# Performance work log

Measured on AMD Instinct MI355X. Metric: run time of the kernel, lower is better.

The kernel has to match this reference:

```python
import jax, jax.numpy as jnp
import numpy as np

N, E, D, L = 50000, 400000, 128, 5
EPS = 1e-5  # BatchNorm1d default eps


def setup_inputs() -> dict:
    key = jax.random.key(0)
    ks = jax.random.split(key, 9)
    x = jax.random.normal(ks[0], (N, D), jnp.float32)
    edge_index = jax.random.randint(ks[1], (2, E), 0, N)
    edge_attr = jax.random.normal(ks[2], (E, 4), jnp.float32)
    # per-layer params (stacked over L layers)
    W1 = jax.random.normal(ks[3], (L, 3, D), jnp.float32) * (6.0 / (3 + D)) ** 0.5
    W2 = jax.random.normal(ks[4], (L, 1, D), jnp.float32) * (6.0 / (1 + D)) ** 0.5
    Wm = jax.random.normal(ks[5], (L, D, 2 * D), jnp.float32) * (6.0 / (3 * D)) ** 0.5
    bm = jnp.zeros((L, D), jnp.float32)
    gamma = jnp.ones((L, D), jnp.float32)
    beta = jnp.zeros((L, D), jnp.float32)
    return dict(x=x, edge_index=edge_index, edge_attr=edge_attr,
                W1=W1, W2=W2, Wm=Wm, bm=bm, gamma=gamma, beta=beta)


def reference(x, edge_index, edge_attr, W1, W2, Wm, bm, gamma, beta):
    row, col = edge_index[0], edge_index[1]
    # symmetric GCN norm: deg computed by scattering ones at col
    deg = jax.ops.segment_sum(jnp.ones((E,), x.dtype), col, num_segments=N)
    deg_safe = jnp.where(deg > 0, deg, 1.0)
    dinv = jnp.where(deg > 0, deg_safe ** -0.5, 0.0)  # [N]
    norm = dinv[row] * dinv[col]                      # [E]

    h = x
    for l in range(L):
        # edge feature projection ('2-3d'): first 3 cols @ W1 + last col @ W2
        edge_fea = edge_attr[:, :3] @ W1[l] + edge_attr[:, 3:] @ W2[l]  # [E, D]
        # message: norm * (x_j + edge_fea), gather at source (row)
        msg = norm[:, None] * (h[row] + edge_fea)                       # [E, D]
        # aggregate: scatter-add at target (col)
        agg = jax.ops.segment_sum(msg, col, num_segments=N)             # [N, D]
        # mlp(concat([x, out])) with ReLU
        h2 = jax.nn.relu(jnp.concatenate([h, agg], axis=1) @ Wm[l].T + bm[l])
        # BatchNorm1d (training mode: batch stats, biased variance)
        mean = h2.mean(axis=0)
        var = jnp.mean((h2 - mean) ** 2, axis=0)
        h = gamma[l] * (h2 - mean) * jax.lax.rsqrt(var + EPS) + beta[l]
        if l < L - 1:
            h = jax.nn.relu(h)
        # dropout p=0 -> identity
    return h
```

## Files before the change

### kernel.cpp

```cpp
#include <hip/hip_runtime.h>

#define D 128
#define EPSBN 1e-5f
#define PB 400
#define GROWS 64
#define GBK 64

typedef __attribute__((ext_vector_type(8))) short bf16x8;
typedef __attribute__((ext_vector_type(4))) float f32x4;

static __device__ __forceinline__ unsigned short f2b(float f) {
    unsigned u = __float_as_uint(f);
    unsigned r = u + 0x7FFF + ((u >> 16) & 1);
    return (unsigned short)(r >> 16);
}
static __device__ __forceinline__ float b2f_lo(unsigned p) { return __uint_as_float(p << 16); }
static __device__ __forceinline__ float b2f_hi(unsigned p) { return __uint_as_float(p & 0xFFFF0000u); }

static __device__ __forceinline__ unsigned short f2h(float f) {
    _Float16 h = (_Float16)f;
    unsigned short u;
    __builtin_memcpy(&u, &h, 2);
    return u;
}
static __device__ __forceinline__ float h2f(unsigned short u) {
    _Float16 h;
    __builtin_memcpy(&h, &u, 2);
    return (float)h;
}
static __device__ __forceinline__ float h2f_lo(unsigned p) { return h2f((unsigned short)(p & 0xFFFF)); }
static __device__ __forceinline__ float h2f_hi(unsigned p) { return h2f((unsigned short)(p >> 16)); }


__global__ void k_deg(const int* __restrict__ ei, int E, int* __restrict__ deg,
                      int* __restrict__ pos) {
    int e = blockIdx.x * 256 + threadIdx.x;
    if (e < E) pos[e] = atomicAdd(&deg[ei[E + e]], 1);
}

__global__ void k_bsum(const int* __restrict__ deg, int* __restrict__ bsum, int N) {
    __shared__ int sm[256];
    int t = threadIdx.x, v = blockIdx.x * 256 + t;
    sm[t] = (v < N) ? deg[v] : 0;
    __syncthreads();
    for (int off = 128; off > 0; off >>= 1) {
        if (t < off) sm[t] += sm[t + off];
        __syncthreads();
    }
    if (t == 0) bsum[blockIdx.x] = sm[0];
}

__global__ void k_bscan(const int* __restrict__ bsum, int* __restrict__ boff,
                        int* __restrict__ row_ptr, int NB, int N, int E) {
    __shared__ int sm[256];
    int t = threadIdx.x;
    int v = (t < NB) ? bsum[t] : 0;
    sm[t] = v;
    __syncthreads();
    for (int off = 1; off < 256; off <<= 1) {
        int x = (t >= off) ? sm[t - off] : 0;
        __syncthreads();
        sm[t] += x;
        __syncthreads();
    }
    if (t < NB) boff[t] = sm[t] - v;
    if (t == 0) row_ptr[N] = E;
}

__global__ void k_scatter(const int* __restrict__ deg, const int* __restrict__ boff,
                          int* __restrict__ row_ptr, int N) {
    __shared__ int sm[256];
    int t = threadIdx.x, v = blockIdx.x * 256 + t;
    int val = (v < N) ? deg[v] : 0;
    sm[t] = val;
    __syncthreads();
    for (int off = 1; off < 256; off <<= 1) {
        int x = (t >= off) ? sm[t - off] : 0;
        __syncthreads();
        sm[t] += x;
        __syncthreads();
    }
    if (v < N) row_ptr[v] = boff[blockIdx.x] + sm[t] - val;
}

__global__ void k_place(const int* __restrict__ ei, const int* __restrict__ row_ptr,
                        const int* __restrict__ pos, int2* __restrict__ csr, int E) {
    int e = blockIdx.x * 256 + threadIdx.x;
    if (e >= E) return;
    int c = ei[E + e];
    csr[row_ptr[c] + pos[e]] = make_int2(ei[e], e);
}

__global__ void k_cvals(const int* __restrict__ row_ptr, int2* __restrict__ csr,
                        const int* __restrict__ deg, const float* __restrict__ attr,
                        float4* __restrict__ cvals, int N) {
    int v = blockIdx.x * 256 + threadIdx.x;
    if (v >= N) return;
    int dgv = deg[v];
    float dv = (dgv > 0) ? rsqrtf((float)dgv) : 0.f;
    int jb = row_ptr[v], je = row_ptr[v + 1];
    float4 acc = make_float4(0.f, 0.f, 0.f, 0.f);
    for (int j = jb; j < je; ++j) {
        int2 e = csr[j];
        int dgs = deg[e.x];
        float ds = (dgs > 0) ? rsqrtf((float)dgs) : 0.f;
        float nm = ds * dv;
        float4 a = *(const float4*)(attr + (size_t)e.y * 4);
        acc.x += nm * a.x; acc.y += nm * a.y;
        acc.z += nm * a.z; acc.w += nm * a.w;
        csr[j] = make_int2(e.x, __float_as_int(nm));
    }
    cvals[v] = acc;
}

__global__ void k_cvt(const float* __restrict__ in, unsigned short* __restrict__ outp, int n4) {
    int i = blockIdx.x * 256 + threadIdx.x;
    if (i >= n4) return;
    float4 v = *(const float4*)(in + (size_t)i * 4);
    ushort4 p;
    p.x = f2b(v.x); p.y = f2b(v.y); p.z = f2b(v.z); p.w = f2b(v.w);
    *(ushort4*)(outp + (size_t)i * 4) = p;
}


__global__ __launch_bounds__(256) void k_spmm(
        const unsigned short* __restrict__ hb, const int* __restrict__ row_ptr,
        const int2* __restrict__ csr, const float4* __restrict__ cvals,
        const float* __restrict__ W1l, const float* __restrict__ W2l,
        const float* __restrict__ scsh, int apply,
        unsigned short* __restrict__ aggb, int N) {
    int lane = threadIdx.x & 63;
    int wave = threadIdx.x >> 6;
    int nh = lane >> 5;
    int v = blockIdx.x * 8 + wave * 2 + nh;
    if (v >= N) return;
    int qw = (lane >> 4) & 1;
    int l4 = lane & 15;
    int d0 = l4 * 8;
    int jb = row_ptr[v], je = row_ptr[v + 1];

    float a[8];
#pragma unroll
    for (int i = 0; i < 8; ++i) a[i] = 0.f;

    if (apply) {
        float sc[8], sh[8];
#pragma unroll
        for (int i = 0; i < 8; i += 4) {
            float4 s = *(const float4*)(scsh + d0 + i);
            float4 t = *(const float4*)(scsh + D + d0 + i);
            sc[i] = s.x; sc[i + 1] = s.y; sc[i + 2] = s.z; sc[i + 3] = s.w;
            sh[i] = t.x; sh[i + 1] = t.y; sh[i + 2] = t.z; sh[i + 3] = t.w;
        }
        for (int j0 = jb; j0 < je; j0 += 4) {
            int ja = j0 + qw, jc = j0 + 2 + qw;
            bool oa = (ja < je), oc = (jc < je);
            int2 ea = csr[oa ? ja : jb];
            int2 ec = csr[oc ? jc : jb];
            float na = oa ? __int_as_float(ea.y) : 0.f;
            float nc = oc ? __int_as_float(ec.y) : 0.f;
            uint4 pa = *(const uint4*)(hb + (size_t)ea.x * D + d0);
            uint4 pc = *(const uint4*)(hb + (size_t)ec.x * D + d0);
            float xa[8] = {h2f_lo(pa.x), h2f_hi(pa.x), h2f_lo(pa.y), h2f_hi(pa.y),
                           h2f_lo(pa.z), h2f_hi(pa.z), h2f_lo(pa.w), h2f_hi(pa.w)};
            float xc[8] = {h2f_lo(pc.x), h2f_hi(pc.x), h2f_lo(pc.y), h2f_hi(pc.y),
                           h2f_lo(pc.z), h2f_hi(pc.z), h2f_lo(pc.w), h2f_hi(pc.w)};
#pragma unroll
            for (int i = 0; i < 8; ++i) {
                a[i] += na * fmaxf(sc[i] * xa[i] + sh[i], 0.f);
                a[i] += nc * fmaxf(sc[i] * xc[i] + sh[i], 0.f);
            }
        }
    } else {
        for (int j0 = jb; j0 < je; j0 += 4) {
            int ja = j0 + qw, jc = j0 + 2 + qw;
            bool oa = (ja < je), oc = (jc < je);
            int2 ea = csr[oa ? ja : jb];
            int2 ec = csr[oc ? jc : jb];
            float na = oa ? __int_as_float(ea.y) : 0.f;
            float nc = oc ? __int_as_float(ec.y) : 0.f;
            uint4 pa = *(const uint4*)(hb + (size_t)ea.x * D + d0);
            uint4 pc = *(const uint4*)(hb + (size_t)ec.x * D + d0);
            a[0] += na * b2f_lo(pa.x) + nc * b2f_lo(pc.x);
            a[1] += na * b2f_hi(pa.x) + nc * b2f_hi(pc.x);
            a[2] += na * b2f_lo(pa.y) + nc * b2f_lo(pc.y);
            a[3] += na * b2f_hi(pa.y) + nc * b2f_hi(pc.y);
            a[4] += na * b2f_lo(pa.z) + nc * b2f_lo(pc.z);
            a[5] += na * b2f_hi(pa.z) + nc * b2f_hi(pc.z);
            a[6] += na * b2f_lo(pa.w) + nc * b2f_lo(pc.w);
            a[7] += na * b2f_hi(pa.w) + nc * b2f_hi(pc.w);
        }
    }
#pragma unroll
    for (int i = 0; i < 8; ++i) a[i] += __shfl_xor(a[i], 16);

    if (qw == 0) {
        float4 c = cvals[v];
        float4 wa0 = *(const float4*)(W1l + d0);
        float4 wa1 = *(const float4*)(W1l + d0 + 4);
        float4 wb0 = *(const float4*)(W1l + D + d0);
        float4 wb1 = *(const float4*)(W1l + D + d0 + 4);
        float4 wc0 = *(const float4*)(W1l + 2 * D + d0);
        float4 wc1 = *(const float4*)(W1l + 2 * D + d0 + 4);
        float4 wd0 = *(const float4*)(W2l + d0);
        float4 wd1 = *(const float4*)(W2l + d0 + 4);
        a[0] += c.x * wa0.x + c.y * wb0.x + c.z * wc0.x + c.w * wd0.x;
        a[1] += c.x * wa0.y + c.y * wb0.y + c.z * wc0.y + c.w * wd0.y;
        a[2] += c.x * wa0.z + c.y * wb0.z + c.z * wc0.z + c.w * wd0.z;
        a[3] += c.x * wa0.w + c.y * wb0.w + c.z * wc0.w + c.w * wd0.w;
        a[4] += c.x * wa1.x + c.y * wb1.x + c.z * wc1.x + c.w * wd1.x;
        a[5] += c.x * wa1.y + c.y * wb1.y + c.z * wc1.y + c.w * wd1.y;
        a[6] += c.x * wa1.z + c.y * wb1.z + c.z * wc1.z + c.w * wd1.z;
        a[7] += c.x * wa1.w + c.y * wb1.w + c.z * wc1.w + c.w * wd1.w;
        uint4 o;
        o.x = ((unsigned)f2b(a[1]) << 16) | (unsigned)f2b(a[0]);
        o.y = ((unsigned)f2b(a[3]) << 16) | (unsigned)f2b(a[2]);
        o.z = ((unsigned)f2b(a[5]) << 16) | (unsigned)f2b(a[4]);
        o.w = ((unsigned)f2b(a[7]) << 16) | (unsigned)f2b(a[6]);
        *(uint4*)(aggb + (size_t)v * D + d0) = o;
    }
}

__global__ __launch_bounds__(256) void k_gemm(
        const unsigned short* __restrict__ hsrc, const unsigned short* __restrict__ aggb,
        const unsigned short* __restrict__ Wmb, const float* __restrict__ bml,
        const float* __restrict__ scsh, int apply,
        unsigned short* __restrict__ h2h, float* __restrict__ pbuf, int N) {
    __shared__ unsigned short As[2][GROWS][GBK + 8];
    __shared__ unsigned short Bs[D][GBK + 8];
    __shared__ float sred[2][4][D];
    int tid = threadIdx.x;
    int lane = tid & 63, wave = tid >> 6;
    int n0a = blockIdx.x * (2 * GROWS);
    int l15 = lane & 15, q = lane >> 4;
    f32x4 acc[2][8];
#pragma unroll
    for (int t2 = 0; t2 < 2; ++t2)
#pragma unroll
        for (int t = 0; t < 8; ++t) acc[t2][t] = (f32x4){0.f, 0.f, 0.f, 0.f};

    for (int kc = 0; kc < 4; ++kc) {
        const unsigned short* src = (kc < 2) ? hsrc : aggb;
        bool aff = (kc < 2) && apply;
        int k0 = (kc & 1) * GBK;
#pragma unroll
        for (int t2 = 0; t2 < 2; ++t2) {
#pragma unroll
            for (int i = 0; i < 2; ++i) {
                int idx = tid + i * 256;
                int r = idx >> 3, seg = idx & 7;
                int m = n0a + t2 * GROWS + r;
                uint4 val = make_uint4(0u, 0u, 0u, 0u);
                if (m < N) val = *(const uint4*)(src + (size_t)m * D + k0 + seg * 8);
                if (aff) {
                    int db = k0 + seg * 8;
                    float4 s0 = *(const float4*)(scsh + db);
                    float4 s1 = *(const float4*)(scsh + db + 4);
                    float4 t0 = *(const float4*)(scsh + D + db);
                    float4 t1 = *(const float4*)(scsh + D + db + 4);
                    float e0 = fmaxf(s0.x * h2f_lo(val.x) + t0.x, 0.f);
                    float e1 = fmaxf(s0.y * h2f_hi(val.x) + t0.y, 0.f);
                    float e2 = fmaxf(s0.z * h2f_lo(val.y) + t0.z, 0.f);
                    float e3 = fmaxf(s0.w * h2f_hi(val.y) + t0.w, 0.f);
                    float e4 = fmaxf(s1.x * h2f_lo(val.z) + t1.x, 0.f);
                    float e5 = fmaxf(s1.y * h2f_hi(val.z) + t1.y, 0.f);
                    float e6 = fmaxf(s1.z * h2f_lo(val.w) + t1.z, 0.f);
                    float e7 = fmaxf(s1.w * h2f_hi(val.w) + t1.w, 0.f);
                    val.x = ((unsigned)f2b(e1) << 16) | (unsigned)f2b(e0);
                    val.y = ((unsigned)f2b(e3) << 16) | (unsigned)f2b(e2);
                    val.z = ((unsigned)f2b(e5) << 16) | (unsigned)f2b(e4);
                    val.w = ((unsigned)f2b(e7) << 16) | (unsigned)f2b(e6);
                }
                *(uint4*)&As[t2][r][seg * 8] = val;
            }
        }
#pragma unroll
        for (int i = 0; i < 4; ++i) {
            int idx = tid + i * 256;
            int n = idx >> 3, seg = idx & 7;
            *(uint4*)&Bs[n][seg * 8] =
                *(const uint4*)(Wmb + (size_t)n * 256 + kc * GBK + seg * 8);
        }
        __syncthreads();
#pragma unroll
        for (int s = 0; s < 2; ++s) {
            bf16x8 a0 = *(const bf16x8*)&As[0][wave * 16 + l15][s * 32 + q * 8];
            bf16x8 a1 = *(const bf16x8*)&As[1][wave * 16 + l15][s * 32 + q * 8];
#pragma unroll
            for (int t = 0; t < 8; ++t) {
                bf16x8 b = *(const bf16x8*)&Bs[t * 16 + l15][s * 32 + q * 8];
                acc[0][t] = __builtin_amdgcn_mfma_f32_16x16x32_bf16(a0, b, acc[0][t], 0, 0, 0);
                acc[1][t] = __builtin_amdgcn_mfma_f32_16x16x32_bf16(a1, b, acc[1][t], 0, 0, 0);
            }
        }
        __syncthreads();
    }
    float ps[8], pq[8];
#pragma unroll
    for (int t = 0; t < 8; ++t) { ps[t] = 0.f; pq[t] = 0.f; }
#pragma unroll
    for (int t2 = 0; t2 < 2; ++t2) {
        int n0 = n0a + t2 * GROWS;
        bool full = (n0 + GROWS <= N);
#pragma unroll
        for (int t = 0; t < 8; ++t) {
            int n = t * 16 + l15;
            float bias = bml[n];
#pragma unroll
            for (int r = 0; r < 4; ++r) {
                int m = n0 + wave * 16 + q * 4 + r;
                float v = fmaxf(acc[t2][t][r] + bias, 0.f);
                if (full || m < N) {
                    h2h[(size_t)m * D + n] = f2h(v);
                    ps[t] += v; pq[t] += v * v;
                }
            }
        }
    }
#pragma unroll
    for (int t = 0; t < 8; ++t) {
        ps[t] += __shfl_xor(ps[t], 16); ps[t] += __shfl_xor(ps[t], 32);
        pq[t] += __shfl_xor(pq[t], 16); pq[t] += __shfl_xor(pq[t], 32);
    }
    if (q == 0) {
#pragma unroll
        for (int t = 0; t < 8; ++t) {
            sred[0][wave][t * 16 + l15] = ps[t];
            sred[1][wave][t * 16 + l15] = pq[t];
        }
    }
    __syncthreads();
    if (tid < D) {
        float s = sred[0][0][tid] + sred[0][1][tid] + sred[0][2][tid] + sred[0][3][tid];
        pbuf[(size_t)tid * PB + blockIdx.x] = s;
    } else {
        int n = tid - D;
        float qv = sred[1][0][n] + sred[1][1][n] + sred[1][2][n] + sred[1][3][n];
        pbuf[(size_t)(n + D) * PB + blockIdx.x] = qv;
    }
}

__global__ __launch_bounds__(128) void k_reduce(
        const float* __restrict__ pbuf, const float* __restrict__ gam,
        const float* __restrict__ bet, float* __restrict__ scsh, int nb, int N) {
    int n = blockIdx.x;
    int t = threadIdx.x;
    float s = 0.f, qv = 0.f;
    for (int b = t; b < nb; b += 128) {
        s  += pbuf[(size_t)n * PB + b];
        qv += pbuf[(size_t)(n + D) * PB + b];
    }
#pragma unroll
    for (int off = 32; off > 0; off >>= 1) {
        s += __shfl_down(s, off);
        qv += __shfl_down(qv, off);
    }
    __shared__ float aux[4];
    if ((t & 63) == 0) { aux[t >> 6] = s; aux[2 + (t >> 6)] = qv; }
    __syncthreads();
    if (t == 0) {
        float S = aux[0] + aux[1], Q = aux[2] + aux[3];
        float mean = S / (float)N;
        float var = fmaxf(Q / (float)N - mean * mean, 0.f);
        float sc = gam[n] * rsqrtf(var + EPSBN);
        scsh[n] = sc;
        scsh[D + n] = bet[n] - mean * sc;
    }
}

__global__ void k_norm_last(const unsigned short* __restrict__ h2h,
                            const float* __restrict__ scsh,
                            float* __restrict__ out_f, int total4) {
    int i = blockIdx.x * 256 + threadIdx.x;
    if (i >= total4) return;
    int base = i * 4;
    int d = base & (D - 1);
    uint2 p = *(const uint2*)(h2h + base);
    float4 o;
    o.x = scsh[d + 0] * h2f_lo(p.x) + scsh[D + d + 0];
    o.y = scsh[d + 1] * h2f_hi(p.x) + scsh[D + d + 1];
    o.z = scsh[d + 2] * h2f_lo(p.y) + scsh[D + d + 2];
    o.w = scsh[d + 3] * h2f_hi(p.y) + scsh[D + d + 3];
    *(float4*)(out_f + base) = o;
}


extern "C" void kernel_launch(void* const* d_in, const int* in_sizes, int n_in,
                              void* d_out, int out_size, void* d_ws, size_t ws_size,
                              hipStream_t stream) {
    const float* x    = (const float*)d_in[0];
    const int*   ei   = (const int*)d_in[1];
    const float* attr = (const float*)d_in[2];
    const float* W1   = (const float*)d_in[3];
    const float* W2   = (const float*)d_in[4];
    const float* Wm   = (const float*)d_in[5];
    const float* bm   = (const float*)d_in[6];
    const float* gam  = (const float*)d_in[7];
    const float* bet  = (const float*)d_in[8];
    float* out = (float*)d_out;

    const int N = in_sizes[0] / D;
    const int E = in_sizes[1] / 2;
    const int L = in_sizes[3] / (3 * D);
    const int NB = (N + 255) / 256;

    size_t off = 0;
    auto carve = [&](size_t bytes) {
        void* p = (char*)d_ws + off;
        off += (bytes + 255) & ~(size_t)255;
        return p;
    };
    int*            deg     = (int*)carve((size_t)N * 4);
    int*            row_ptr = (int*)carve((size_t)(N + 1) * 4);
    int*            pos     = (int*)carve((size_t)E * 4);
    int*            bsum    = (int*)carve((size_t)NB * 4);
    int*            boff    = (int*)carve((size_t)NB * 4);
    int2*           csr     = (int2*)carve((size_t)(E + 8) * 8);
    float4*         cvals   = (float4*)carve((size_t)N * 16);
    unsigned short* xb      = (unsigned short*)carve((size_t)N * D * 2);
    unsigned short* h2h     = (unsigned short*)carve((size_t)N * D * 2);
    unsigned short* aggb    = (unsigned short*)carve((size_t)N * D * 2);
    unsigned short* Wmb     = (unsigned short*)carve((size_t)L * D * 256 * 2);
    float*          pbuf    = (float*)carve((size_t)2 * D * PB * 4);
    float*          scsh    = (float*)carve((size_t)2 * D * 4);
    (void)ws_size;

    hipMemsetAsync(deg, 0, (size_t)N * 4, stream);

    const int eb = (E + 255) / 256;
    k_deg<<<eb, 256, 0, stream>>>(ei, E, deg, pos);
    k_bsum<<<NB, 256, 0, stream>>>(deg, bsum, N);
    k_bscan<<<1, 256, 0, stream>>>(bsum, boff, row_ptr, NB, N, E);
    k_scatter<<<NB, 256, 0, stream>>>(deg, boff, row_ptr, N);
    k_place<<<eb, 256, 0, stream>>>(ei, row_ptr, pos, csr, E);
    k_cvals<<<NB, 256, 0, stream>>>(row_ptr, csr, deg, attr, cvals, N);

    const int xq = N * D / 4;
    k_cvt<<<(xq + 255) / 256, 256, 0, stream>>>(x, xb, xq);
    const int wq = L * D * 256 / 4;
    k_cvt<<<(wq + 255) / 256, 256, 0, stream>>>(Wm, Wmb, wq);

    const int total4 = N * D / 4;
    const int gemmb = (N + 2 * GROWS - 1) / (2 * GROWS);
    const int spmmb = (N + 7) / 8;

    for (int l = 0; l < L; ++l) {
        const unsigned short* in = (l == 0) ? xb : h2h;
        const int apply = (l > 0) ? 1 : 0;
        const float* W1l = W1 + (size_t)l * 3 * D;
        const float* W2l = W2 + (size_t)l * D;
        const unsigned short* Wml = Wmb + (size_t)l * D * 256;
        const float* bml = bm + (size_t)l * D;

        k_spmm<<<spmmb, 256, 0, stream>>>(in, row_ptr, csr, cvals, W1l, W2l,
                                          scsh, apply, aggb, N);
        k_gemm<<<gemmb, 256, 0, stream>>>(in, aggb, Wml, bml, scsh, apply,
                                          h2h, pbuf, N);
        k_reduce<<<D, 128, 0, stream>>>(pbuf, gam + (size_t)l * D,
                                        bet + (size_t)l * D, scsh, gemmb, N);
    }
    k_norm_last<<<(total4 + 255) / 256, 256, 0, stream>>>(h2h, scsh, out, total4);
}
```

Before: 388.9 us.

## Replace BN reduce kernel with atomic stats and inline scale/shift computation

After: 419.6 us. 7.9% more time.

```diff
diff --git a/kernel.cpp b/kernel.cpp
--- a/kernel.cpp
+++ b/kernel.cpp
@@ -2,7 +2,6 @@
 
 #define D 128
 #define EPSBN 1e-5f
-#define PB 400
 #define GROWS 64
 #define GBK 64
 
@@ -127,8 +126,10 @@
         const unsigned short* __restrict__ hb, const int* __restrict__ row_ptr,
         const int2* __restrict__ csr, const float4* __restrict__ cvals,
         const float* __restrict__ W1l, const float* __restrict__ W2l,
-        const float* __restrict__ scsh, int apply,
-        unsigned short* __restrict__ aggb, int N) {
+        const float* __restrict__ stats_prev, float* __restrict__ stats_cur,
+        const float* __restrict__ gam_p, const float* __restrict__ bet_p,
+        int apply, unsigned short* __restrict__ aggb, int N) {
+    if (blockIdx.x == 0) stats_cur[threadIdx.x] = 0.f;
     int lane = threadIdx.x & 63;
     int wave = threadIdx.x >> 6;
     int nh = lane >> 5;
@@ -145,50 +146,56 @@
 
     if (apply) {
         float sc[8], sh[8];
-#pragma unroll
-        for (int i = 0; i < 8; i += 4) {
-            float4 s = *(const float4*)(scsh + d0 + i);
-            float4 t = *(const float4*)(scsh + D + d0 + i);
-            sc[i] = s.x; sc[i + 1] = s.y; sc[i + 2] = s.z; sc[i + 3] = s.w;
-            sh[i] = t.x; sh[i + 1] = t.y; sh[i + 2] = t.z; sh[i + 3] = t.w;
-        }
-        for (int j0 = jb; j0 < je; j0 += 4) {
-            int ja = j0 + qw, jc = j0 + 2 + qw;
-            bool oa = (ja < je), oc = (jc < je);
-            int2 ea = csr[oa ? ja : jb];
-            int2 ec = csr[oc ? jc : jb];
-            float na = oa ? __int_as_float(ea.y) : 0.f;
-            float nc = oc ? __int_as_float(ec.y) : 0.f;
-            uint4 pa = *(const uint4*)(hb + (size_t)ea.x * D + d0);
-            uint4 pc = *(const uint4*)(hb + (size_t)ec.x * D + d0);
-            float xa[8] = {h2f_lo(pa.x), h2f_hi(pa.x), h2f_lo(pa.y), h2f_hi(pa.y),
-                           h2f_lo(pa.z), h2f_hi(pa.z), h2f_lo(pa.w), h2f_hi(pa.w)};
-            float xc[8] = {h2f_lo(pc.x), h2f_hi(pc.x), h2f_lo(pc.y), h2f_hi(pc.y),
-                           h2f_lo(pc.z), h2f_hi(pc.z), h2f_lo(pc.w), h2f_hi(pc.w)};
-#pragma unroll
-            for (int i = 0; i < 8; ++i) {
-                a[i] += na * fmaxf(sc[i] * xa[i] + sh[i], 0.f);
-                a[i] += nc * fmaxf(sc[i] * xc[i] + sh[i], 0.f);
+        float rn = 1.0f / (float)N;
+#pragma unroll
+        for (int i = 0; i < 8; ++i) {
+            int n = d0 + i;
+            float mean = stats_prev[n] * rn;
+            float var = fmaxf(stats_prev[D + n] * rn - mean * mean, 0.f);
+            sc[i] = gam_p[n] * rsqrtf(var + EPSBN);
+            sh[i] = bet_p[n] - mean * sc[i];
+        }
+        for (int j0 = jb; j0 < je; j0 += 8) {
+            int2 e[4]; float nm[4]; uint4 p[4];
+#pragma unroll
+            for (int s = 0; s < 4; ++s) {
+                int j = j0 + 2 * s + qw;
+                bool ok = (j < je);
+                e[s] = csr[ok ? j : jb];
+                nm[s] = ok ? __int_as_float(e[s].y) : 0.f;
+            }
+#pragma unroll
+            for (int s = 0; s < 4; ++s)
+                p[s] = *(const uint4*)(hb + (size_t)e[s].x * D + d0);
+#pragma unroll
+            for (int s = 0; s < 4; ++s) {
+                float xv[8] = {h2f_lo(p[s].x), h2f_hi(p[s].x), h2f_lo(p[s].y), h2f_hi(p[s].y),
+                               h2f_lo(p[s].z), h2f_hi(p[s].z), h2f_lo(p[s].w), h2f_hi(p[s].w)};
+#pragma unroll
+                for (int i = 0; i < 8; ++i)
+                    a[i] += nm[s] * fmaxf(sc[i] * xv[i] + sh[i], 0.f);
             }
         }
     } else {
-        for (int j0 = jb; j0 < je; j0 += 4) {
-            int ja = j0 + qw, jc = j0 + 2 + qw;
-            bool oa = (ja < je), oc = (jc < je);
-            int2 ea = csr[oa ? ja : jb];
-            int2 ec = csr[oc ? jc : jb];
-            float na = oa ? __int_as_float(ea.y) : 0.f;
-            float nc = oc ? __int_as_float(ec.y) : 0.f;
-            uint4 pa = *(const uint4*)(hb + (size_t)ea.x * D + d0);
-            uint4 pc = *(const uint4*)(hb + (size_t)ec.x * D + d0);
-            a[0] += na * b2f_lo(pa.x) + nc * b2f_lo(pc.x);
-            a[1] += na * b2f_hi(pa.x) + nc * b2f_hi(pc.x);
-            a[2] += na * b2f_lo(pa.y) + nc * b2f_lo(pc.y);
-            a[3] += na * b2f_hi(pa.y) + nc * b2f_hi(pc.y);
-            a[4] += na * b2f_lo(pa.z) + nc * b2f_lo(pc.z);
-            a[5] += na * b2f_hi(pa.z) + nc * b2f_hi(pc.z);
-            a[6] += na * b2f_lo(pa.w) + nc * b2f_lo(pc.w);
-            a[7] += na * b2f_hi(pa.w) + nc * b2f_hi(pc.w);
+        for (int j0 = jb; j0 < je; j0 += 8) {
+            int2 e[4]; float nm[4]; uint4 p[4];
+#pragma unroll
+            for (int s = 0; s < 4; ++s) {
+                int j = j0 + 2 * s + qw;
+                bool ok = (j < je);
+                e[s] = csr[ok ? j : jb];
+                nm[s] = ok ? __int_as_float(e[s].y) : 0.f;
+            }
+#pragma unroll
+            for (int s = 0; s < 4; ++s)
+                p[s] = *(const uint4*)(hb + (size_t)e[s].x * D + d0);
+#pragma unroll
+            for (int s = 0; s < 4; ++s) {
+                a[0] += nm[s] * b2f_lo(p[s].x); a[1] += nm[s] * b2f_hi(p[s].x);
+                a[2] += nm[s] * b2f_lo(p[s].y); a[3] += nm[s] * b2f_hi(p[s].y);
+                a[4] += nm[s] * b2f_lo(p[s].z); a[5] += nm[s] * b2f_hi(p[s].z);
+                a[6] += nm[s] * b2f_lo(p[s].w); a[7] += nm[s] * b2f_hi(p[s].w);
+            }
         }
     }
 #pragma unroll
@@ -224,15 +231,28 @@
 __global__ __launch_bounds__(256) void k_gemm(
         const unsigned short* __restrict__ hsrc, const unsigned short* __restrict__ aggb,
         const unsigned short* __restrict__ Wmb, const float* __restrict__ bml,
-        const float* __restrict__ scsh, int apply,
-        unsigned short* __restrict__ h2h, float* __restrict__ pbuf, int N) {
+        const float* __restrict__ stats_prev, float* __restrict__ stats_cur,
+        const float* __restrict__ gam_p, const float* __restrict__ bet_p,
+        int apply, unsigned short* __restrict__ h2h, int N) {
     __shared__ unsigned short As[2][GROWS][GBK + 8];
     __shared__ unsigned short Bs[D][GBK + 8];
     __shared__ float sred[2][4][D];
+    __shared__ float scsh_l[2 * D];
     int tid = threadIdx.x;
     int lane = tid & 63, wave = tid >> 6;
     int n0a = blockIdx.x * (2 * GROWS);
     int l15 = lane & 15, q = lane >> 4;
+
+    if (apply && tid < D) {
+        float rn = 1.0f / (float)N;
+        float mean = stats_prev[tid] * rn;
+        float var = fmaxf(stats_prev[D + tid] * rn - mean * mean, 0.f);
+        float sc = gam_p[tid] * rsqrtf(var + EPSBN);
+        scsh_l[tid] = sc;
+        scsh_l[D + tid] = bet_p[tid] - mean * sc;
+    }
+    if (apply) __syncthreads();
+
     f32x4 acc[2][8];
 #pragma unroll
     for (int t2 = 0; t2 < 2; ++t2)
@@ -254,10 +274,10 @@
                 if (m < N) val = *(const uint4*)(src + (size_t)m * D + k0 + seg * 8);
                 if (aff) {
                     int db = k0 + seg * 8;
-                    float4 s0 = *(const float4*)(scsh + db);
-                    float4 s1 = *(const float4*)(scsh + db + 4);
-                    float4 t0 = *(const float4*)(scsh + D + db);
-                    float4 t1 = *(const float4*)(scsh + D + db + 4);
+                    float4 s0 = *(const float4*)(scsh_l + db);
+                    float4 s1 = *(const float4*)(scsh_l + db + 4);
+                    float4 t0 = *(const float4*)(scsh_l + D + db);
+                    float4 t1 = *(const float4*)(scsh_l + D + db + 4);
                     float e0 = fmaxf(s0.x * h2f_lo(val.x) + t0.x, 0.f);
                     float e1 = fmaxf(s0.y * h2f_hi(val.x) + t0.y, 0.f);
                     float e2 = fmaxf(s0.z * h2f_lo(val.y) + t0.z, 0.f);
@@ -332,55 +352,38 @@
     __syncthreads();
     if (tid < D) {
         float s = sred[0][0][tid] + sred[0][1][tid] + sred[0][2][tid] + sred[0][3][tid];
-        pbuf[(size_t)tid * PB + blockIdx.x] = s;
+        atomicAdd(&stats_cur[tid], s);
     } else {
         int n = tid - D;
         float qv = sred[1][0][n] + sred[1][1][n] + sred[1][2][n] + sred[1][3][n];
-        pbuf[(size_t)(n + D) * PB + blockIdx.x] = qv;
-    }
-}
-
-__global__ __launch_bounds__(128) void k_reduce(
-        const float* __restrict__ pbuf, const float* __restrict__ gam,
-        const float* __restrict__ bet, float* __restrict__ scsh, int nb, int N) {
-    int n = blockIdx.x;
-    int t = threadIdx.x;
-    float s = 0.f, qv = 0.f;
-    for (int b = t; b < nb; b += 128) {
-        s  += pbuf[(size_t)n * PB + b];
-        qv += pbuf[(size_t)(n + D) * PB + b];
-    }
-#pragma unroll
-    for (int off = 32; off > 0; off >>= 1) {
-        s += __shfl_down(s, off);
-        qv += __shfl_down(qv, off);
-    }
-    __shared__ float aux[4];
-    if ((t & 63) == 0) { aux[t >> 6] = s; aux[2 + (t >> 6)] = qv; }
-    __syncthreads();
-    if (t == 0) {
-        float S = aux[0] + aux[1], Q = aux[2] + aux[3];
-        float mean = S / (float)N;
-        float var = fmaxf(Q / (float)N - mean * mean, 0.f);
-        float sc = gam[n] * rsqrtf(var + EPSBN);
-        scsh[n] = sc;
-        scsh[D + n] = bet[n] - mean * sc;
+        atomicAdd(&stats_cur[D + n], qv);
     }
 }
 
 __global__ void k_norm_last(const unsigned short* __restrict__ h2h,
-                            const float* __restrict__ scsh,
-                            float* __restrict__ out_f, int total4) {
+                            const float* __restrict__ stats,
+                            const float* __restrict__ gam_p, const float* __restrict__ bet_p,
+                            float* __restrict__ out_f, int total4, int N) {
     int i = blockIdx.x * 256 + threadIdx.x;
     if (i >= total4) return;
     int base = i * 4;
     int d = base & (D - 1);
+    float rn = 1.0f / (float)N;
+    float sc[4], sh[4];
+#pragma unroll
+    for (int k = 0; k < 4; ++k) {
+        int n = d + k;
+        float mean = stats[n] * rn;
+        float var = fmaxf(stats[D + n] * rn - mean * mean, 0.f);
+        sc[k] = gam_p[n] * rsqrtf(var + EPSBN);
+        sh[k] = bet_p[n] - mean * sc[k];
+    }
     uint2 p = *(const uint2*)(h2h + base);
     float4 o;
-    o.x = scsh[d + 0] * h2f_lo(p.x) + scsh[D + d + 0];
-    o.y = scsh[d + 1] * h2f_hi(p.x) + scsh[D + d + 1];
-    o.z = scsh[d + 2] * h2f_lo(p.y) + scsh[D + d + 2];
-    o.w = scsh[d + 3] * h2f_hi(p.y) + scsh[D + d + 3];
+    o.x = sc[0] * h2f_lo(p.x) + sh[0];
+    o.y = sc[1] * h2f_hi(p.x) + sh[1];
+    o.z = sc[2] * h2f_lo(p.y) + sh[2];
+    o.w = sc[3] * h2f_hi(p.y) + sh[3];
     *(float4*)(out_f + base) = o;
 }
 
@@ -421,8 +424,7 @@
     unsigned short* h2h     = (unsigned short*)carve((size_t)N * D * 2);
     unsigned short* aggb    = (unsigned short*)carve((size_t)N * D * 2);
     unsigned short* Wmb     = (unsigned short*)carve((size_t)L * D * 256 * 2);
-    float*          pbuf    = (float*)carve((size_t)2 * D * PB * 4);
-    float*          scsh    = (float*)carve((size_t)2 * D * 4);
+    float*          stats   = (float*)carve((size_t)2 * 2 * D * 4);
     (void)ws_size;
 
     hipMemsetAsync(deg, 0, (size_t)N * 4, stream);
@@ -451,13 +453,19 @@
         const float* W2l = W2 + (size_t)l * D;
         const unsigned short* Wml = Wmb + (size_t)l * D * 256;
         const float* bml = bm + (size_t)l * D;
+        float* stats_cur = stats + (size_t)(l & 1) * 2 * D;
+        const float* stats_prev = stats + (size_t)((l ^ 1) & 1) * 2 * D;
+        const float* gam_p = gam + (size_t)(l > 0 ? l - 1 : 0) * D;
+        const float* bet_p = bet + (size_t)(l > 0 ? l - 1 : 0) * D;
 
         k_spmm<<<spmmb, 256, 0, stream>>>(in, row_ptr, csr, cvals, W1l, W2l,
-                                          scsh, apply, aggb, N);
-        k_gemm<<<gemmb, 256, 0, stream>>>(in, aggb, Wml, bml, scsh, apply,
-                                          h2h, pbuf, N);
-        k_reduce<<<D, 128, 0, stream>>>(pbuf, gam + (size_t)l * D,
-                                        bet + (size_t)l * D, scsh, gemmb, N);
-    }
-    k_norm_last<<<(total4 + 255) / 256, 256, 0, stream>>>(h2h, scsh, out, total4);
-}
+                                          stats_prev, stats_cur, gam_p, bet_p,
+                                          apply, aggb, N);
+        k_gemm<<<gemmb, 256, 0, stream>>>(in, aggb, Wml, bml,
+                                          stats_prev, stats_cur, gam_p, bet_p,
+                                          apply, h2h, N);
+    }
+    k_norm_last<<<(total4 + 255) / 256, 256, 0, stream>>>(
+        h2h, stats + (size_t)((L - 1) & 1) * 2 * D,
+        gam + (size_t)(L - 1) * D, bet + (size_t)(L - 1) * D, out, total4, N);
+}
```
